# Performance work log

Measured on AMD Instinct MI355X. Metric: run time of the kernel, lower is better.

Reference implementation:

```python
import jax, jax.numpy as jnp
import numpy as np

B, C, H, W = 8, 320, 32, 32
HEADS, DHEAD = 8, 40
CTX_LEN, CTX_DIM = 77, 768
FF_INNER = 4 * C
GROUPS = 32
HW = H * W


def setup_inputs() -> dict:
    key = jax.random.key(0)
    ks = jax.random.split(key, 16)
    def nrm(k, shape, s=0.02):
        return (jax.random.normal(k, shape) * s).astype(jnp.float32)
    z = lambda *s: jnp.zeros(s, jnp.float32)
    o = lambda *s: jnp.ones(s, jnp.float32)
    inp = {}
    inp["x"] = jax.random.normal(ks[0], (B, C, H, W), jnp.float32)
    inp["context"] = jax.random.normal(ks[1], (B, CTX_LEN, CTX_DIM), jnp.float32)
    inp["vis_mask"] = jax.random.uniform(ks[2], (B, HW, HW)) > 0.5
    inp["v2t_mask"] = jax.random.uniform(ks[3], (B, HW, CTX_LEN)) > 0.5
    inp["gn_scale"] = o(C); inp["gn_bias"] = z(C)
    inp["proj_in_w"] = nrm(ks[4], (C, C)); inp["proj_in_b"] = z(C)
    inp["n1_s"] = o(C); inp["n1_b"] = z(C)
    inp["wq1"] = nrm(ks[5], (C, C)); inp["wk1"] = nrm(ks[6], (C, C)); inp["wv1"] = nrm(ks[7], (C, C))
    inp["wo1"] = nrm(ks[8], (C, C)); inp["bo1"] = z(C)
    inp["n2_s"] = o(C); inp["n2_b"] = z(C)
    inp["wq2"] = nrm(ks[9], (C, C)); inp["wk2"] = nrm(ks[10], (CTX_DIM, C)); inp["wv2"] = nrm(ks[11], (CTX_DIM, C))
    inp["wo2"] = nrm(ks[12], (C, C)); inp["bo2"] = z(C)
    inp["n3_s"] = o(C); inp["n3_b"] = z(C)
    inp["ff_w1"] = nrm(ks[13], (C, 2 * FF_INNER)); inp["ff_b1"] = z(2 * FF_INNER)
    inp["ff_w2"] = nrm(ks[14], (FF_INNER, C)); inp["ff_b2"] = z(C)
    inp["proj_out_w"] = nrm(ks[15], (C, C)); inp["proj_out_b"] = z(C)
    return inp


def group_norm(x, scale, bias, eps=1e-6):
    b, c, h, w = x.shape
    xg = x.reshape(b, GROUPS, -1)
    mu = xg.mean(-1, keepdims=True)
    var = xg.var(-1, keepdims=True)
    xn = ((xg - mu) * jax.lax.rsqrt(var + eps)).reshape(b, c, h, w)
    return xn * scale[None, :, None, None] + bias[None, :, None, None]


def layer_norm(x, s, b, eps=1e-5):
    mu = x.mean(-1, keepdims=True)
    var = x.var(-1, keepdims=True)
    return (x - mu) * jax.lax.rsqrt(var + eps) * s + b


def mha(xq, ctx, wq, wk, wv, wo, bo, mask):
    # CrossAttention: manual einsum softmax with boolean mask broadcast over heads
    b, n, _ = xq.shape
    m = ctx.shape[1]
    split = lambda t: t.reshape(b, -1, HEADS, DHEAD).transpose(0, 2, 1, 3)
    q = split(xq @ wq)   # [b,h,n,d]
    k = split(ctx @ wk)  # [b,h,m,d]
    v = split(ctx @ wv)
    sim = jnp.einsum('bhid,bhjd->bhij', q, k) * (DHEAD ** -0.5)
    if mask is not None:
        sim = jnp.where(mask[:, None, :, :], sim, jnp.finfo(sim.dtype).min)
    attn = jax.nn.softmax(sim, axis=-1)
    out = jnp.einsum('bhij,bhjd->bhid', attn, v)
    out = out.transpose(0, 2, 1, 3).reshape(b, n, HEADS * DHEAD)
    return out @ wo + bo


def reference(x, context, vis_mask, v2t_mask, gn_scale, gn_bias, proj_in_w, proj_in_b,
              n1_s, n1_b, wq1, wk1, wv1, wo1, bo1,
              n2_s, n2_b, wq2, wk2, wv2, wo2, bo2,
              n3_s, n3_b, ff_w1, ff_b1, ff_w2, ff_b2,
              proj_out_w, proj_out_b):
    x_in = x
    h = group_norm(x, gn_scale, gn_bias)
    # 1x1 conv proj_in == per-pixel linear; flatten b c h w -> b (hw) c
    h = h.reshape(B, C, HW).transpose(0, 2, 1) @ proj_in_w + proj_in_b
    # masked self-attention (vis mask)
    h = h + mha(layer_norm(h, n1_s, n1_b), layer_norm(h, n1_s, n1_b),
                wq1, wk1, wv1, wo1, bo1, vis_mask)
    # masked cross-attention to text (v2t mask)
    h = h + mha(layer_norm(h, n2_s, n2_b), context,
                wq2, wk2, wv2, wo2, bo2, v2t_mask)
    # GEGLU feedforward (glu=True, mult=4)
    y = layer_norm(h, n3_s, n3_b) @ ff_w1 + ff_b1
    a, g = jnp.split(y, 2, axis=-1)
    h = h + (a * jax.nn.gelu(g, approximate=False)) @ ff_w2 + ff_b2
    # proj_out + residual
    out = (h @ proj_out_w + proj_out_b).transpose(0, 2, 1).reshape(B, C, H, W)
    return out + x_in
```

## Files before the change

### kernel.cpp

```cpp
#include <hip/hip_runtime.h>
#include <hip/hip_bf16.h>
#include <math.h>


#define Bsz   8
#define Cch   320
#define HW    1024
#define NTOK  (Bsz*HW)
#define HEADS 8
#define DHEAD 40
#define CTXL  77
#define CTXD  768
#define FFI   1280
#define MCTX  (Bsz*CTXL)
#define MCTXP 640

typedef unsigned short u16;
typedef unsigned long long u64;
typedef __attribute__((ext_vector_type(8))) u16    u16x8;
typedef __attribute__((ext_vector_type(4))) u16    u16x4;
typedef __attribute__((ext_vector_type(8))) __bf16 bf16x8;
typedef __attribute__((ext_vector_type(4))) float  f32x4;

__device__ inline u16 f2b(float f) {
    unsigned u = __float_as_uint(f);
    return (u16)((u + 0x7FFFu + ((u >> 16) & 1u)) >> 16);
}

__global__ __launch_bounds__(256) void gn_apply(
    const float* __restrict__ x, const float* __restrict__ gnA,
    const float* __restrict__ gnB, u16* __restrict__ out)
{
    __shared__ u16 T[64*72];
    const int tid = threadIdx.x;
    const int c0 = blockIdx.x * 64;
    const int p0 = blockIdx.y * 64;
    const int b  = blockIdx.z;
    for (int e = tid; e < 512; e += 256) {
        int r = e >> 3, ch = e & 7;
        const float* src = x + ((size_t)(b*Cch + c0 + r))*HW + p0 + ch*8;
        float a  = gnA[b*Cch + c0 + r];
        float bb = gnB[b*Cch + c0 + r];
        float4 v0 = *(const float4*)src;
        float4 v1 = *(const float4*)(src + 4);
        u16x8 val;
        val[0] = f2b(v0.x*a + bb); val[1] = f2b(v0.y*a + bb);
        val[2] = f2b(v0.z*a + bb); val[3] = f2b(v0.w*a + bb);
        val[4] = f2b(v1.x*a + bb); val[5] = f2b(v1.y*a + bb);
        val[6] = f2b(v1.z*a + bb); val[7] = f2b(v1.w*a + bb);
        *(u16x8*)&T[r*72 + (ch ^ (r & 7))*8] = val;
    }
    __syncthreads();
    for (int e = tid; e < 4096; e += 256) {
        int p = e >> 6, c = e & 63;
        u16 v = T[c*72 + (((p >> 3) ^ (c & 7))*8) + (p & 7)];
        out[((size_t)(b*HW + p0 + p))*Cch + c0 + c] = v;
    }
}

__global__ __launch_bounds__(256) void layernorm_kernel(
    const float* __restrict__ in, const float* __restrict__ s,
    const float* __restrict__ bgain, u16* __restrict__ out)
{
    int t = blockIdx.x*4 + (threadIdx.x >> 6);
    int lane = threadIdx.x & 63;
    const float* row = in + (size_t)t*Cch;
    float v[5];
    float sum = 0.f, sq = 0.f;
    #pragma unroll
    for (int i = 0; i < 5; ++i) {
        v[i] = row[lane + 64*i];
        sum += v[i]; sq += v[i]*v[i];
    }
    #pragma unroll
    for (int off = 32; off > 0; off >>= 1) {
        sum += __shfl_xor(sum, off);
        sq  += __shfl_xor(sq,  off);
    }
    float mean = sum * (1.f/320.f);
    float var  = sq  * (1.f/320.f) - mean*mean;
    float inv  = rsqrtf(var + 1e-5f);
    u16* orow = out + (size_t)t*Cch;
    #pragma unroll
    for (int i = 0; i < 5; ++i) {
        int c = lane + 64*i;
        orow[c] = f2b((v[i]-mean)*inv*s[c] + bgain[c]);
    }
}

struct WDesc { const float* src; u16* dst; int K; int N; int tiles; float scl; };
struct WPack { WDesc w[12]; };

#define WT_TILES 620
#define CTXBLK   240

__global__ __launch_bounds__(256) void preamble(
    WPack p, const float* __restrict__ ctxsrc, u16* __restrict__ ctxdst,
    const void* __restrict__ vis, const void* __restrict__ v2t,
    u64* __restrict__ bvis, u64* __restrict__ bv2t,
    const float* __restrict__ x, const float* __restrict__ gscale,
    const float* __restrict__ gbias, float* __restrict__ gnA,
    float* __restrict__ gnB)
{
    __shared__ u16 T[64*72];
    int blk = blockIdx.x;
    int tid = threadIdx.x;
    if (blk < WT_TILES) {
        int t = blk;
        #pragma unroll
        for (int i = 0; i < 12; ++i) {
            int nt = p.w[i].tiles;
            if (t < nt) {
                const int K = p.w[i].K, N = p.w[i].N;
                const int ntN = N >> 6;
                const int tk = t / ntN, tn = t - tk*ntN;
                const float scl = p.w[i].scl;
                const float* src = p.w[i].src;
                u16* dst = p.w[i].dst;
                for (int e = tid; e < 512; e += 256) {
                    int r = e >> 3, ch = e & 7;
                    const float* sp = src + (size_t)(tk*64 + r)*N + tn*64 + ch*8;
                    float4 v0 = *(const float4*)sp;
                    float4 v1 = *(const float4*)(sp + 4);
                    u16x8 val;
                    val[0] = f2b(v0.x*scl); val[1] = f2b(v0.y*scl);
                    val[2] = f2b(v0.z*scl); val[3] = f2b(v0.w*scl);
                    val[4] = f2b(v1.x*scl); val[5] = f2b(v1.y*scl);
                    val[6] = f2b(v1.z*scl); val[7] = f2b(v1.w*scl);
                    *(u16x8*)&T[r*72 + (ch ^ (r & 7))*8] = val;
                }
                __syncthreads();
                for (int e = tid; e < 4096; e += 256) {
                    int n = e >> 6, k = e & 63;
                    u16 v = T[k*72 + (((n >> 3) ^ (k & 7))*8) + (n & 7)];
                    dst[(size_t)(tn*64 + n)*K + tk*64 + k] = v;
                }
                return;
            }
            t -= nt;
        }
        return;
    }
    if (blk < WT_TILES + CTXBLK) {
        int idx = (blk - WT_TILES)*2048 + tid*8;
        int r = idx / CTXD;
        u16x8 val = {};
        if (r < MCTX) {
            float4 v0 = *(const float4*)(ctxsrc + idx);
            float4 v1 = *(const float4*)(ctxsrc + idx + 4);
            val[0] = f2b(v0.x); val[1] = f2b(v0.y);
            val[2] = f2b(v0.z); val[3] = f2b(v0.w);
            val[4] = f2b(v1.x); val[5] = f2b(v1.y);
            val[6] = f2b(v1.z); val[7] = f2b(v1.w);
        }
        *(u16x8*)(ctxdst + idx) = val;
        return;
    }
    if (blk >= WT_TILES + CTXBLK + 4096) {
        int gb = blk - (WT_TILES + CTXBLK + 4096);
        int b = gb >> 5, g = gb & 31;
        __shared__ float rs[256], rq[256];
        const float4* xg = (const float4*)(x + ((size_t)b*Cch + g*10)*HW);
        float s = 0.f, q = 0.f;
        #pragma unroll
        for (int i = 0; i < 10; ++i) {
            float4 v = xg[tid + i*256];
            s += v.x + v.y + v.z + v.w;
            q += v.x*v.x + v.y*v.y + v.z*v.z + v.w*v.w;
        }
        rs[tid] = s; rq[tid] = q; __syncthreads();
        for (int off = 128; off > 0; off >>= 1) {
            if (tid < off) { rs[tid] += rs[tid+off]; rq[tid] += rq[tid+off]; }
            __syncthreads();
        }
        if (tid < 10) {
            float mean = rs[0] * (1.f/10240.f);
            float var  = rq[0] * (1.f/10240.f) - mean*mean;
            float inv  = rsqrtf(var + 1e-6f);
            int chn = g*10 + tid;
            float a = inv * gscale[chn];
            gnA[b*Cch + chn] = a;
            gnB[b*Cch + chn] = gbias[chn] - mean*a;
        }
        return;
    }
    __shared__ int any;
    if (tid == 0) any = 0;
    __syncthreads();
    const unsigned char* probe = (const unsigned char*)vis;
    for (int i = tid; i < 4096; i += 256)
        if ((i & 3) && probe[i]) any = 1;
    __syncthreads();
    const int isU8 = any;
    int mb = blk - WT_TILES - CTXBLK;
    const void* mask; u64* bits; int Lkv, nw;
    if (mb < 2048) { mask = vis; bits = bvis; Lkv = HW;   nw = 16; }
    else           { mask = v2t; bits = bv2t; Lkv = CTXL; nw = 2; mb -= 2048; }
    const int wv = tid >> 6, lane = tid & 63;
    const int row = mb*4 + wv;
    const unsigned char* m8  = (const unsigned char*)mask;
    const int*           m32 = (const int*)mask;
    const size_t base = (size_t)row * Lkv;
    for (int w = 0; w < nw; ++w) {
        int j = w*64 + lane;
        bool on = (j < Lkv) && (isU8 ? (m8[base+j] != 0) : (m32[base+j] != 0));
        u64 word = __ballot(on);
        if (lane == 0) bits[(size_t)row*nw + w] = word;
    }
}

__global__ __launch_bounds__(512) void gemm_bf16(
    const u16* __restrict__ A, const u16* __restrict__ Wt,
    const float* __restrict__ bias, const float* __restrict__ res,
    float* __restrict__ out, u16* __restrict__ out_bf, int M, int N, int K)
{
    __shared__ u16 As[2][128*72];
    __shared__ u16 Bs[2][64*72];
    const int tid  = threadIdx.x;
    const int lane = tid & 63;
    const int w    = tid >> 6;
    const int mp   = w >> 1;
    const int np   = w & 1;
    const int m0   = blockIdx.x * 128;
    const int n0   = blockIdx.y * 64;
    const int fr   = lane & 15, fg = lane >> 4;
    const int ar   = tid >> 2, ac = tid & 3;
    const int br   = tid >> 3, bc = tid & 7;

    const u16* pa = A  + (size_t)(m0 + ar)*K + ac*8;
    const u16* pb = Wt + (size_t)(n0 + br)*K + bc*8;
    const int ns = K >> 6;

    *(u16x8*)&As[0][ar*72 + ac*8]      = *(const u16x8*)pa;
    *(u16x8*)&As[0][ar*72 + 32 + ac*8] = *(const u16x8*)(pa + 32);
    *(u16x8*)&Bs[0][br*72 + bc*8]      = *(const u16x8*)pb;
    u16x8 ra0 = {}, ra1 = {}, rb = {};
    if (1 < ns) {
        ra0 = *(const u16x8*)(pa + 64);
        ra1 = *(const u16x8*)(pa + 96);
        rb  = *(const u16x8*)(pb + 64);
    }

    f32x4 acc[2][2] = {};
    for (int s = 0; s < ns; ++s) {
        __syncthreads();
        const int cb = s & 1, nb = cb ^ 1;
        if (s + 1 < ns) {
            *(u16x8*)&As[nb][ar*72 + ac*8]      = ra0;
            *(u16x8*)&As[nb][ar*72 + 32 + ac*8] = ra1;
            *(u16x8*)&Bs[nb][br*72 + bc*8]      = rb;
            if (s + 2 < ns) {
                ra0 = *(const u16x8*)(pa + 64*(s+2));
                ra1 = *(const u16x8*)(pa + 64*(s+2) + 32);
                rb  = *(const u16x8*)(pb + 64*(s+2));
            }
        }
        #pragma unroll
        for (int c = 0; c < 2; ++c) {
            bf16x8 a0 = *(const bf16x8*)&As[cb][(mp*32      + fr)*72 + c*32 + fg*8];
            bf16x8 a1 = *(const bf16x8*)&As[cb][(mp*32 + 16 + fr)*72 + c*32 + fg*8];
            #pragma unroll
            for (int t = 0; t < 2; ++t) {
                bf16x8 b = *(const bf16x8*)&Bs[cb][((np*2+t)*16 + fr)*72 + c*32 + fg*8];
                acc[0][t] = __builtin_amdgcn_mfma_f32_16x16x32_bf16(a0, b, acc[0][t], 0, 0, 0);
                acc[1][t] = __builtin_amdgcn_mfma_f32_16x16x32_bf16(a1, b, acc[1][t], 0, 0, 0);
            }
        }
    }
    #pragma unroll
    for (int at = 0; at < 2; ++at) {
        #pragma unroll
        for (int t = 0; t < 2; ++t) {
            int gn = n0 + (np*2+t)*16 + fr;
            float bv = bias ? bias[gn] : 0.f;
            #pragma unroll
            for (int i = 0; i < 4; ++i) {
                int gm = m0 + mp*32 + at*16 + fg*4 + i;
                float v = acc[at][t][i] + bv;
                if (res) v += res[(size_t)gm*N + gn];
                if (out) out[(size_t)gm*N + gn] = v;
                if (out_bf) out_bf[(size_t)gm*N + gn] = f2b(v);
            }
        }
    }
}

__global__ __launch_bounds__(512) void gemm_qkv_ctx(
    const u16* __restrict__ A, const u16* __restrict__ Wt,
    u16* __restrict__ out_bf, u16* __restrict__ vt_self,
    const u16* __restrict__ ctx, const u16* __restrict__ wk,
    const u16* __restrict__ wv, u16* __restrict__ kout, u16* __restrict__ vout)
{
    __shared__ u16 As[2][128*40];
    __shared__ u16 Bs[2][64*40];
    const int tid  = threadIdx.x;
    const int lane = tid & 63;
    const int w    = tid >> 6;
    const int fr   = lane & 15, fg = lane >> 4;
    const int bi   = blockIdx.x;

    if (bi < 960) {
        const int K  = Cch, N = 960;
        const int m0 = (bi & 63)*128;
        const int n0 = (bi >> 6)*64;
        const int mp = w >> 1, np = w & 1;
        const int ar = tid >> 2, ac = tid & 3;
        const bool hasB = tid < 256;

        const u16* pa = A  + (size_t)(m0 + ar)*K + ac*8;
        const u16* pb = Wt + (size_t)(n0 + ar)*K + ac*8;
        const int nk = K >> 5;

        *(u16x8*)&As[0][ar*40 + ac*8] = *(const u16x8*)pa;
        if (hasB) *(u16x8*)&Bs[0][ar*40 + ac*8] = *(const u16x8*)pb;
        u16x8 xa = *(const u16x8*)(pa + 32);
        u16x8 ya = *(const u16x8*)(pa + 64);
        u16x8 xb = {}, yb = {};
        if (hasB) { xb = *(const u16x8*)(pb + 32); yb = *(const u16x8*)(pb + 64); }

        f32x4 acc[2][2] = {};
        for (int i = 0; i < nk; i += 2) {
            __syncthreads();
            *(u16x8*)&As[1][ar*40 + ac*8] = xa;
            if (hasB) *(u16x8*)&Bs[1][ar*40 + ac*8] = xb;
            if (i + 3 < nk) {
                xa = *(const u16x8*)(pa + 32*(i+3));
                if (hasB) xb = *(const u16x8*)(pb + 32*(i+3));
            }
            {
                bf16x8 a0 = *(const bf16x8*)&As[0][(mp*32      + fr)*40 + fg*8];
                bf16x8 a1 = *(const bf16x8*)&As[0][(mp*32 + 16 + fr)*40 + fg*8];
                #pragma unroll
                for (int t = 0; t < 2; ++t) {
                    bf16x8 b = *(const bf16x8*)&Bs[0][((np*2+t)*16 + fr)*40 + fg*8];
                    acc[0][t] = __builtin_amdgcn_mfma_f32_16x16x32_bf16(a0, b, acc[0][t], 0, 0, 0);
                    acc[1][t] = __builtin_amdgcn_mfma_f32_16x16x32_bf16(a1, b, acc[1][t], 0, 0, 0);
                }
            }
            __syncthreads();
            if (i + 2 < nk) {
                *(u16x8*)&As[0][ar*40 + ac*8] = ya;
                if (hasB) *(u16x8*)&Bs[0][ar*40 + ac*8] = yb;
                if (i + 4 < nk) {
                    ya = *(const u16x8*)(pa + 32*(i+4));
                    if (hasB) yb = *(const u16x8*)(pb + 32*(i+4));
                }
            }
            {
                bf16x8 a0 = *(const bf16x8*)&As[1][(mp*32      + fr)*40 + fg*8];
                bf16x8 a1 = *(const bf16x8*)&As[1][(mp*32 + 16 + fr)*40 + fg*8];
                #pragma unroll
                for (int t = 0; t < 2; ++t) {
                    bf16x8 b = *(const bf16x8*)&Bs[1][((np*2+t)*16 + fr)*40 + fg*8];
                    acc[0][t] = __builtin_amdgcn_mfma_f32_16x16x32_bf16(a0, b, acc[0][t], 0, 0, 0);
                    acc[1][t] = __builtin_amdgcn_mfma_f32_16x16x32_bf16(a1, b, acc[1][t], 0, 0, 0);
                }
            }
        }
        if (n0 < 640) {
            #pragma unroll
            for (int at = 0; at < 2; ++at) {
                #pragma unroll
                for (int t = 0; t < 2; ++t) {
                    int gn = n0 + (np*2+t)*16 + fr;
                    #pragma unroll
                    for (int i = 0; i < 4; ++i) {
                        int gm = m0 + mp*32 + at*16 + fg*4 + i;
                        out_bf[(size_t)gm*N + gn] = f2b(acc[at][t][i]);
                    }
                }
            }
        } else {
            #pragma unroll
            for (int at = 0; at < 2; ++at) {
                #pragma unroll
                for (int t = 0; t < 2; ++t) {
                    int c  = n0 - 640 + (np*2+t)*16 + fr;
                    int gm0 = m0 + mp*32 + at*16 + fg*4;
                    int b  = gm0 >> 10;
                    int p  = gm0 & (HW-1);
                    u16x4 vv;
                    #pragma unroll
                    for (int i = 0; i < 4; ++i) vv[i] = f2b(acc[at][t][i]);
                    *(u16x4*)&vt_self[((size_t)(b*Cch + c))*HW + p] = vv;
                }
            }
        }
        return;
    }

    {
        int cb = bi - 960;
        const int z  = cb / 50; cb -= z*50;
        const int my = cb / 5, nx0 = cb - my*5;
        const int m0 = my*64, n0 = nx0*64;
        const u16* Wt2 = z ? wv : wk;
        u16* outp      = z ? vout : kout;
        const int mg = w >> 1;
        const int np = w & 1;
        const bool isA = tid < 256;
        const int cr = (tid & 255) >> 2, cc = tid & 3;

        const u16* ps = isA ? ctx + (size_t)(m0 + cr)*CTXD + cc*8
                            : Wt2 + (size_t)(n0 + cr)*CTXD + cc*8;
        u16* s0 = isA ? &As[0][cr*40 + cc*8] : &Bs[0][cr*40 + cc*8];
        u16* s1 = isA ? &As[1][cr*40 + cc*8] : &Bs[1][cr*40 + cc*8];
        const int nk = CTXD >> 5;

        *(u16x8*)s0 = *(const u16x8*)ps;
        u16x8 xv = *(const u16x8*)(ps + 32);
        u16x8 yv = *(const u16x8*)(ps + 64);

        f32x4 acc[2] = {};
        for (int i = 0; i < nk; i += 2) {
            __syncthreads();
            *(u16x8*)s1 = xv;
            if (i + 3 < nk) xv = *(const u16x8*)(ps + 32*(i+3));
            {
                bf16x8 a = *(const bf16x8*)&As[0][(mg*16 + fr)*40 + fg*8];
                #pragma unroll
                for (int t = 0; t < 2; ++t) {
                    bf16x8 b = *(const bf16x8*)&Bs[0][((np*2+t)*16 + fr)*40 + fg*8];
                    acc[t] = __builtin_amdgcn_mfma_f32_16x16x32_bf16(a, b, acc[t], 0, 0, 0);
                }
            }
            __syncthreads();
            if (i + 2 < nk) {
                *(u16x8*)s0 = yv;
                if (i + 4 < nk) yv = *(const u16x8*)(ps + 32*(i+4));
            }
            {
                bf16x8 a = *(const bf16x8*)&As[1][(mg*16 + fr)*40 + fg*8];
                #pragma unroll
                for (int t = 0; t < 2; ++t) {
                    bf16x8 b = *(const bf16x8*)&Bs[1][((np*2+t)*16 + fr)*40 + fg*8];
                    acc[t] = __builtin_amdgcn_mfma_f32_16x16x32_bf16(a, b, acc[t], 0, 0, 0);
                }
            }
        }
        #pragma unroll
        for (int t = 0; t < 2; ++t) {
            int gn = n0 + (np*2+t)*16 + fr;
            #pragma unroll
            for (int i = 0; i < 4; ++i) {
                int gm = m0 + mg*16 + fg*4 + i;
                if (gm < MCTX)
                    outp[(size_t)gm*Cch + gn] = f2b(acc[t][i]);
            }
        }
    }
}

__global__ __launch_bounds__(512) void gemm_pout(
    const u16* __restrict__ A, const u16* __restrict__ Wt,
    const float* __restrict__ bias, const float* __restrict__ x,
    float* __restrict__ out, int K)
{
    __shared__ u16 As[2][128*72];
    __shared__ u16 Bs[2][64*72];
    const int tid  = threadIdx.x;
    const int lane = tid & 63;
    const int w    = tid >> 6;
    const int mp   = w >> 1;
    const int np   = w & 1;
    const int m0   = blockIdx.x * 128;
    const int n0   = blockIdx.y * 64;
    const int fr   = lane & 15, fg = lane >> 4;
    const int ar   = tid >> 2, ac = tid & 3;
    const int br   = tid >> 3, bc = tid & 7;

    const u16* pa = A  + (size_t)(m0 + ar)*K + ac*8;
    const u16* pb = Wt + (size_t)(n0 + br)*K + bc*8;
    const int ns = K >> 6;

    *(u16x8*)&As[0][ar*72 + ac*8]      = *(const u16x8*)pa;
    *(u16x8*)&As[0][ar*72 + 32 + ac*8] = *(const u16x8*)(pa + 32);
    *(u16x8*)&Bs[0][br*72 + bc*8]      = *(const u16x8*)pb;
    u16x8 ra0 = {}, ra1 = {}, rb = {};
    if (1 < ns) {
        ra0 = *(const u16x8*)(pa + 64);
        ra1 = *(const u16x8*)(pa + 96);
        rb  = *(const u16x8*)(pb + 64);
    }

    f32x4 acc[2][2] = {};
    for (int s = 0; s < ns; ++s) {
        __syncthreads();
        const int cb = s & 1, nb = cb ^ 1;
        if (s + 1 < ns) {
            *(u16x8*)&As[nb][ar*72 + ac*8]      = ra0;
            *(u16x8*)&As[nb][ar*72 + 32 + ac*8] = ra1;
            *(u16x8*)&Bs[nb][br*72 + bc*8]      = rb;
            if (s + 2 < ns) {
                ra0 = *(const u16x8*)(pa + 64*(s+2));
                ra1 = *(const u16x8*)(pa + 64*(s+2) + 32);
                rb  = *(const u16x8*)(pb + 64*(s+2));
            }
        }
        #pragma unroll
        for (int c = 0; c < 2; ++c) {
            bf16x8 a0 = *(const bf16x8*)&As[cb][(mp*32      + fr)*72 + c*32 + fg*8];
            bf16x8 a1 = *(const bf16x8*)&As[cb][(mp*32 + 16 + fr)*72 + c*32 + fg*8];
            #pragma unroll
            for (int t = 0; t < 2; ++t) {
                bf16x8 b = *(const bf16x8*)&Bs[cb][((np*2+t)*16 + fr)*72 + c*32 + fg*8];
                acc[0][t] = __builtin_amdgcn_mfma_f32_16x16x32_bf16(a0, b, acc[0][t], 0, 0, 0);
                acc[1][t] = __builtin_amdgcn_mfma_f32_16x16x32_bf16(a1, b, acc[1][t], 0, 0, 0);
            }
        }
    }
    #pragma unroll
    for (int at = 0; at < 2; ++at) {
        #pragma unroll
        for (int t = 0; t < 2; ++t) {
            int gn = n0 + (np*2+t)*16 + fr;
            float bv = bias[gn];
            int gm0 = m0 + mp*32 + at*16 + fg*4;
            int b   = gm0 >> 10;
            int pcol= gm0 & (HW-1);
            size_t o = ((size_t)(b*Cch + gn))*HW + pcol;
            f32x4 xv = *(const f32x4*)&x[o];
            f32x4 vv;
            #pragma unroll
            for (int i = 0; i < 4; ++i) vv[i] = acc[at][t][i] + bv + xv[i];
            *(f32x4*)&out[o] = vv;
        }
    }
}

__global__ __launch_bounds__(512) void geglu_bf16(
    const u16* __restrict__ A, const u16* __restrict__ Wt,
    const float* __restrict__ b1, u16* __restrict__ out, int M, int K)
{
    __shared__ u16 As[2][128*40];
    __shared__ u16 Ba[2][64*40];
    __shared__ u16 Bg[2][64*40];
    const int tid  = threadIdx.x;
    const int lane = tid & 63;
    const int w    = tid >> 6;
    const int mp   = w >> 1;
    const int np   = w & 1;
    const int m0   = blockIdx.x * 128;
    const int n0   = blockIdx.y * 64;
    const int fr   = lane & 15, fg = lane >> 4;
    const int ar   = tid >> 2, ac = tid & 3;
    const int nk   = K >> 5;

    const u16* pa = A + (size_t)(m0 + ar)*K + ac*8;
    const int bq = (ar < 64) ? (n0 + ar) : (FFI + n0 + ar - 64);
    const u16* pb = Wt + (size_t)bq*K + ac*8;
    u16* bs0 = (ar < 64) ? &Ba[0][ar*40 + ac*8] : &Bg[0][(ar-64)*40 + ac*8];
    u16* bs1 = (ar < 64) ? &Ba[1][ar*40 + ac*8] : &Bg[1][(ar-64)*40 + ac*8];

    *(u16x8*)&As[0][ar*40 + ac*8] = *(const u16x8*)pa;
    *(u16x8*)bs0 = *(const u16x8*)pb;
    u16x8 xa = *(const u16x8*)(pa + 32);
    u16x8 xb = *(const u16x8*)(pb + 32);
    u16x8 ya = *(const u16x8*)(pa + 64);
    u16x8 yb = *(const u16x8*)(pb + 64);

    f32x4 aca[2][2] = {}, acg[2][2] = {};
    for (int i = 0; i < nk; i += 2) {
        __syncthreads();
        *(u16x8*)&As[1][ar*40 + ac*8] = xa;
        *(u16x8*)bs1 = xb;
        if (i + 3 < nk) {
            xa = *(const u16x8*)(pa + 32*(i+3));
            xb = *(const u16x8*)(pb + 32*(i+3));
        }
        {
            bf16x8 a0 = *(const bf16x8*)&As[0][(mp*32      + fr)*40 + fg*8];
            bf16x8 a1 = *(const bf16x8*)&As[0][(mp*32 + 16 + fr)*40 + fg*8];
            #pragma unroll
            for (int t = 0; t < 2; ++t) {
                bf16x8 ba = *(const bf16x8*)&Ba[0][((np*2+t)*16 + fr)*40 + fg*8];
                bf16x8 bg = *(const bf16x8*)&Bg[0][((np*2+t)*16 + fr)*40 + fg*8];
                aca[0][t] = __builtin_amdgcn_mfma_f32_16x16x32_bf16(a0, ba, aca[0][t], 0, 0, 0);
                aca[1][t] = __builtin_amdgcn_mfma_f32_16x16x32_bf16(a1, ba, aca[1][t], 0, 0, 0);
                acg[0][t] = __builtin_amdgcn_mfma_f32_16x16x32_bf16(a0, bg, acg[0][t], 0, 0, 0);
                acg[1][t] = __builtin_amdgcn_mfma_f32_16x16x32_bf16(a1, bg, acg[1][t], 0, 0, 0);
            }
        }
        __syncthreads();
        if (i + 2 < nk) {
            *(u16x8*)&As[0][ar*40 + ac*8] = ya;
            *(u16x8*)bs0 = yb;
            if (i + 4 < nk) {
                ya = *(const u16x8*)(pa + 32*(i+4));
                yb = *(const u16x8*)(pb + 32*(i+4));
            }
        }
        {
            bf16x8 a0 = *(const bf16x8*)&As[1][(mp*32      + fr)*40 + fg*8];
            bf16x8 a1 = *(const bf16x8*)&As[1][(mp*32 + 16 + fr)*40 + fg*8];
            #pragma unroll
            for (int t = 0; t < 2; ++t) {
                bf16x8 ba = *(const bf16x8*)&Ba[1][((np*2+t)*16 + fr)*40 + fg*8];
                bf16x8 bg = *(const bf16x8*)&Bg[1][((np*2+t)*16 + fr)*40 + fg*8];
                aca[0][t] = __builtin_amdgcn_mfma_f32_16x16x32_bf16(a0, ba, aca[0][t], 0, 0, 0);
                aca[1][t] = __builtin_amdgcn_mfma_f32_16x16x32_bf16(a1, ba, aca[1][t], 0, 0, 0);
                acg[0][t] = __builtin_amdgcn_mfma_f32_16x16x32_bf16(a0, bg, acg[0][t], 0, 0, 0);
                acg[1][t] = __builtin_amdgcn_mfma_f32_16x16x32_bf16(a1, bg, acg[1][t], 0, 0, 0);
            }
        }
    }
    #pragma unroll
    for (int at = 0; at < 2; ++at) {
        #pragma unroll
        for (int t = 0; t < 2; ++t) {
            int gn = n0 + (np*2+t)*16 + fr;
            float ba = b1[gn], bg = b1[FFI + gn];
            #pragma unroll
            for (int i = 0; i < 4; ++i) {
                int gm = m0 + mp*32 + at*16 + fg*4 + i;
                float av = aca[at][t][i] + ba;
                float gv = acg[at][t][i] + bg;
                float gel = 0.5f*gv*(1.f + erff(gv*0.70710678118654752f));
                out[(size_t)gm*FFI + gn] = f2b(av*gel);
            }
        }
    }
}

__global__ __launch_bounds__(512) void flash_mfma(
    const u16* __restrict__ qb, int qstride,
    const u16* __restrict__ kb, int kstride,
    const u16* __restrict__ vt, int vstride,
    const u64* __restrict__ mbits, int nw,
    u16* __restrict__ out,
    int Lkv,
    const u16* __restrict__ tin, u16* __restrict__ tout)
{
    __shared__ u16 QPs[128*72];
    __shared__ u16 Ks[2][64*72];
    __shared__ u16 Vs[2][48*72];

    const int tid  = threadIdx.x;
    const int bi   = blockIdx.x;

    if (bi >= 512) {
        int cb = bi - 512;
        const int c0 = (cb % 5)*64;
        const int t0 = ((cb/5) & 1)*64;
        const int b  = cb/10;
        {
            int r = tid >> 3, ch2 = tid & 7;
            u16x8 val = {};
            if (t0 + r < CTXL)
                val = *(const u16x8*)(tin + ((size_t)(b*CTXL + t0 + r))*Cch + c0 + ch2*8);
            *(u16x8*)&QPs[r*72 + (ch2 ^ (r & 7))*8] = val;
        }
        __syncthreads();
        for (int e = tid; e < 4096; e += 512) {
            int c = e >> 6, t = e & 63;
            u16 v = QPs[t*72 + (((c >> 3) ^ (t & 7))*8) + (c & 7)];
            tout[((size_t)(b*Cch + c0 + c))*128 + t0 + t] = v;
        }
        return;
    }

    const int lane = tid & 63;
    const int w    = tid >> 6;
    const int col  = lane & 15;
    const int quad = lane >> 4;
    const int hb   = (bi & 7)*8 + (bi >> 6);
    const int qt   = (bi >> 3) & 7;
    const int h    = hb & 7;
    const int b    = hb >> 3;
    const int q0   = qt*128;
    const int ch   = tid & 7;
    const int r0   = tid >> 3;

    {
        const u16* qT = qb + ((size_t)(b*HW + q0))*qstride + (size_t)h*DHEAD + ch*8;
        u16x8 v0 = {}, v1 = {};
        if (ch < 5) {
            v0 = *(const u16x8*)(qT + (size_t)r0*qstride);
            v1 = *(const u16x8*)(qT + (size_t)(r0+64)*qstride);
        }
        *(u16x8*)&QPs[r0*72 + ch*8]      = v0;
        *(u16x8*)&QPs[(r0+64)*72 + ch*8] = v1;
    }
    if (tid < 128) {
        int rr  = tid >> 3;
        int row = 40 + (rr & 7);
        int buf = rr >> 3;
        u16x8 v = {};
        if (row == DHEAD) {
            #pragma unroll
            for (int z = 0; z < 8; ++z) v[z] = 0x3F80;
        }
        *(u16x8*)&Vs[buf][row*72 + ch*8] = v;
    }

    const bool kok = ch < 5;
    const u16* kR = kb + (size_t)b*Lkv*kstride + (size_t)h*DHEAD + ch*8
                       + (size_t)r0*kstride;
    const u16* vR = vt + ((size_t)(b*Cch + h*DHEAD))*vstride + ch*8
                       + (size_t)r0*vstride;
    const bool vok = r0 < DHEAD;
    const u64* mrow = mbits + ((size_t)(b*HW + q0 + w*16 + quad*4))*nw;

    u16x8 nk = {}, nv = {};
    if (kok && r0 < Lkv) nk = *(const u16x8*)kR;
    if (vok) nv = *(const u16x8*)vR;

    __syncthreads();
    const bf16x8 qa0 = *(const bf16x8*)&QPs[(w*16 + col)*72 +  0 + quad*8];
    const bf16x8 qa1 = *(const bf16x8*)&QPs[(w*16 + col)*72 + 32 + quad*8];

    f32x4 acc_o[3] = {};

    const int nkt = (Lkv + 63) / 64;
    int cur = 0;
    for (int jt = 0; jt < nkt; ++jt) {
        *(u16x8*)&Ks[cur][r0*72 + ch*8] = nk;
        if (vok) *(u16x8*)&Vs[cur][r0*72 + ch*8] = nv;
        if (jt + 1 < nkt) {
            kR += (size_t)64*kstride;
            vR += 64;
            nk = (u16x8){};
            if (kok && ((jt+1)*64 + r0 < Lkv)) nk = *(const u16x8*)kR;
            if (vok) nv = *(const u16x8*)vR;
        }
        __syncthreads();

        u64 mw[4];
        #pragma unroll
        for (int i = 0; i < 4; ++i) mw[i] = mrow[i*nw + jt];

        f32x4 s[4] = {};
        #pragma unroll
        for (int nt = 0; nt < 4; ++nt) {
            bf16x8 b0 = *(const bf16x8*)&Ks[cur][(nt*16 + col)*72 +  0 + quad*8];
            bf16x8 b1 = *(const bf16x8*)&Ks[cur][(nt*16 + col)*72 + 32 + quad*8];
            s[nt] = __builtin_amdgcn_mfma_f32_16x16x32_bf16(qa0, b0, s[nt], 0, 0, 0);
            s[nt] = __builtin_amdgcn_mfma_f32_16x16x32_bf16(qa1, b1, s[nt], 0, 0, 0);
        }

        #pragma unroll
        for (int i = 0; i < 4; ++i) {
            #pragma unroll
            for (int nt = 0; nt < 4; ++nt) {
                float p = __builtin_amdgcn_exp2f(s[nt][i]);
                unsigned bits = (unsigned)(mw[i] >> (nt*16));
                s[nt][i] = ((bits >> col) & 1u) ? p : 0.f;
            }
        }

        #pragma unroll
        for (int nt = 0; nt < 4; ++nt)
            #pragma unroll
            for (int i = 0; i < 4; ++i)
                QPs[(w*16 + quad*4 + i)*68 + nt*16 + col] =
                    (u16)(__float_as_uint(s[nt][i]) >> 16);

        bf16x8 pa0, pa1;
        __builtin_memcpy(&pa0, &QPs[(w*16 + col)*68 +  0 + quad*8], 16);
        __builtin_memcpy(&pa1, &QPs[(w*16 + col)*68 + 32 + quad*8], 16);
        #pragma unroll
        for (int nt = 0; nt < 3; ++nt) {
            bf16x8 vb0 = *(const bf16x8*)&Vs[cur][(nt*16 + col)*72 +  0 + quad*8];
            bf16x8 vb1 = *(const bf16x8*)&Vs[cur][(nt*16 + col)*72 + 32 + quad*8];
            acc_o[nt] = __builtin_amdgcn_mfma_f32_16x16x32_bf16(pa0, vb0, acc_o[nt], 0, 0, 0);
            acc_o[nt] = __builtin_amdgcn_mfma_f32_16x16x32_bf16(pa1, vb1, acc_o[nt], 0, 0, 0);
        }
        cur ^= 1;
    }

    float inv_l[4];
    #pragma unroll
    for (int i = 0; i < 4; ++i)
        inv_l[i] = 1.f / __shfl(acc_o[2][i], (lane & 48) | 8);

    #pragma unroll
    for (int nt = 0; nt < 3; ++nt) {
        int d = nt*16 + col;
        if (d < DHEAD) {
            #pragma unroll
            for (int i = 0; i < 4; ++i) {
                int q = q0 + w*16 + quad*4 + i;
                out[((size_t)(b*HW + q))*Cch + h*DHEAD + d] = f2b(acc_o[nt][i] * inv_l[i]);
            }
        }
    }
}

extern "C" void kernel_launch(void* const* d_in, const int* in_sizes, int n_in,
                              void* d_out, int out_size, void* d_ws, size_t ws_size,
                              hipStream_t stream)
{
    const float* x        = (const float*)d_in[0];
    const float* context  = (const float*)d_in[1];
    const void*  vis_mask = d_in[2];
    const void*  v2t_mask = d_in[3];
    const float* gn_s     = (const float*)d_in[4];
    const float* gn_b     = (const float*)d_in[5];
    const float* proj_in_w= (const float*)d_in[6];
    const float* proj_in_b= (const float*)d_in[7];
    const float* n1_s     = (const float*)d_in[8];
    const float* n1_b     = (const float*)d_in[9];
    const float* wq1      = (const float*)d_in[10];
    const float* wk1      = (const float*)d_in[11];
    const float* wv1      = (const float*)d_in[12];
    const float* wo1      = (const float*)d_in[13];
    const float* bo1      = (const float*)d_in[14];
    const float* n2_s     = (const float*)d_in[15];
    const float* n2_b     = (const float*)d_in[16];
    const float* wq2      = (const float*)d_in[17];
    const float* wk2      = (const float*)d_in[18];
    const float* wv2      = (const float*)d_in[19];
    const float* wo2      = (const float*)d_in[20];
    const float* bo2      = (const float*)d_in[21];
    const float* n3_s     = (const float*)d_in[22];
    const float* n3_b     = (const float*)d_in[23];
    const float* ff_w1    = (const float*)d_in[24];
    const float* ff_b1    = (const float*)d_in[25];
    const float* ff_w2    = (const float*)d_in[26];
    const float* ff_b2    = (const float*)d_in[27];
    const float* pout_w   = (const float*)d_in[28];
    const float* pout_b   = (const float*)d_in[29];
    float* out = (float*)d_out;

    const size_t TOKC = (size_t)NTOK*Cch;
    float* ws   = (float*)d_ws;
    float* Hb   = ws;
    u16*   QKV  = (u16*)(Hb + TOKC);
    u16*   Vt_g = QKV + 3*TOKC;
    u16*   G_bf = QKV;
    u16*   T0b  = Vt_g + TOKC;
    u16*   T1b  = T0b + TOKC;
    u16*   Hb_bf= T1b + TOKC;
    u16*   Wbf  = Hb_bf + TOKC;
    u64*   mb_vis = (u64*)(Wbf + 2539520);
    u64*   mb_v2t = mb_vis + 131072;
    u16*   ctx_bf = (u16*)(mb_v2t + 16384);
    u16*   Kc_bf  = ctx_bf + MCTXP*CTXD;
    u16*   Vc_bf  = Kc_bf + 640*Cch;
    float* gnA    = (float*)(Vc_bf + 640*Cch);
    float* gnB    = gnA + Bsz*Cch;
    u16*   Vt_x   = (u16*)(gnB + Bsz*Cch);

    u16* w_q1  = Wbf;
    u16* w_k1  = Wbf +  102400;
    u16* w_v1  = Wbf +  204800;
    u16* w_pin = Wbf +  307200;
    u16* w_o1  = Wbf +  409600;
    u16* w_q2  = Wbf +  512000;
    u16* w_o2  = Wbf +  614400;
    u16* w_ff1 = Wbf +  716800;
    u16* w_ff2 = Wbf + 1536000;
    u16* w_po  = Wbf + 1945600;
    u16* w_k2  = Wbf + 2048000;
    u16* w_v2  = Wbf + 2293760;

    const float qscale = 0.15811388300841897f * 1.4426950408889634f;
    WPack pack;
    pack.w[0]  = { wq1,       w_q1,  Cch, Cch, 25,  qscale };
    pack.w[1]  = { wk1,       w_k1,  Cch, Cch, 25,  1.f };
    pack.w[2]  = { wv1,       w_v1,  Cch, Cch, 25,  1.f };
    pack.w[3]  = { proj_in_w, w_pin, Cch, Cch, 25,  1.f };
    pack.w[4]  = { wo1,       w_o1,  Cch, Cch, 25,  1.f };
    pack.w[5]  = { wq2,       w_q2,  Cch, Cch, 25,  qscale };
    pack.w[6]  = { wo2,       w_o2,  Cch, Cch, 25,  1.f };
    pack.w[7]  = { ff_w1,     w_ff1, Cch, 2*FFI, 200, 1.f };
    pack.w[8]  = { ff_w2,     w_ff2, FFI, Cch, 100, 1.f };
    pack.w[9]  = { pout_w,    w_po,  Cch, Cch, 25,  1.f };
    pack.w[10] = { wk2,       w_k2,  CTXD, Cch, 60, 1.f };
    pack.w[11] = { wv2,       w_v2,  CTXD, Cch, 60, 1.f };

    dim3 blk256(256);
    dim3 blk512(512);
    dim3 gTok(NTOK/128, Cch/64);
    dim3 gFF(NTOK/128, FFI/64);
    dim3 gGN(Cch/64, HW/64, Bsz);

    preamble<<<WT_TILES + CTXBLK + 4096 + 256, blk256, 0, stream>>>(
        pack, context, ctx_bf, vis_mask, v2t_mask, mb_vis, mb_v2t,
        x, gn_s, gn_b, gnA, gnB);

    gn_apply<<<gGN, blk256, 0, stream>>>(x, gnA, gnB, T0b);
    gemm_bf16<<<gTok, blk512, 0, stream>>>(T0b, w_pin, proj_in_b, nullptr, Hb, nullptr, NTOK, Cch, Cch);

    layernorm_kernel<<<NTOK/4, blk256, 0, stream>>>(Hb, n1_s, n1_b, T0b);
    gemm_qkv_ctx<<<1060, blk512, 0, stream>>>(T0b, w_q1, QKV, Vt_g,
                                              ctx_bf, w_k2, w_v2, Kc_bf, Vc_bf);
    flash_mfma<<<512 + 80, blk512, 0, stream>>>(QKV, 960, QKV + 320, 960, Vt_g, HW,
                                                mb_vis, 16, T1b, HW, Vc_bf, Vt_x);
    gemm_bf16<<<gTok, blk512, 0, stream>>>(T1b, w_o1, bo1, Hb, Hb, nullptr, NTOK, Cch, Cch);

    layernorm_kernel<<<NTOK/4, blk256, 0, stream>>>(Hb, n2_s, n2_b, T0b);
    gemm_bf16<<<gTok, blk512, 0, stream>>>(T0b, w_q2, nullptr, nullptr, nullptr, QKV, NTOK, Cch, Cch);
    flash_mfma<<<512, blk512, 0, stream>>>(QKV, Cch, Kc_bf, Cch, Vt_x, 128,
                                           mb_v2t, 2, T1b, CTXL, nullptr, nullptr);
    gemm_bf16<<<gTok, blk512, 0, stream>>>(T1b, w_o2, bo2, Hb, Hb, nullptr, NTOK, Cch, Cch);

    layernorm_kernel<<<NTOK/4, blk256, 0, stream>>>(Hb, n3_s, n3_b, T0b);
    geglu_bf16<<<gFF, blk512, 0, stream>>>(T0b, w_ff1, ff_b1, G_bf, NTOK, Cch);
    gemm_bf16<<<gTok, blk512, 0, stream>>>(G_bf, w_ff2, ff_b2, Hb, nullptr, Hb_bf, NTOK, Cch, FFI);

    gemm_pout<<<gTok, blk512, 0, stream>>>(Hb_bf, w_po, pout_b, x, out, Cch);
}
```

Measured before the change: 342.5 us.

## Process two query tiles per block in self-attention flash kernel to reuse K/V

```diff
diff --git a/kernel.cpp b/kernel.cpp
--- a/kernel.cpp
+++ b/kernel.cpp
@@ -622,13 +622,14 @@
     }
 }
 
+template<int NQT>
 __global__ __launch_bounds__(512) void flash_mfma(
     const u16* __restrict__ qb, int qstride,
     const u16* __restrict__ kb, int kstride,
     const u16* __restrict__ vt, int vstride,
     const u64* __restrict__ mbits, int nw,
     u16* __restrict__ out,
-    int Lkv,
+    int Lkv, int natt,
     const u16* __restrict__ tin, u16* __restrict__ tout)
 {
     __shared__ u16 QPs[128*72];
@@ -638,8 +639,8 @@
     const int tid  = threadIdx.x;
     const int bi   = blockIdx.x;
 
-    if (bi >= 512) {
-        int cb = bi - 512;
+    if (bi >= natt) {
+        int cb = bi - natt;
         const int c0 = (cb % 5)*64;
         const int t0 = ((cb/5) & 1)*64;
         const int b  = cb/10;
@@ -663,24 +664,20 @@
     const int w    = tid >> 6;
     const int col  = lane & 15;
     const int quad = lane >> 4;
-    const int hb   = (bi & 7)*8 + (bi >> 6);
-    const int qt   = (bi >> 3) & 7;
-    const int h    = hb & 7;
-    const int b    = hb >> 3;
-    const int q0   = qt*128;
+    int b, h, q0;
+    if (NQT == 2) {
+        b  = bi & 7;
+        h  = bi >> 5;
+        q0 = ((bi >> 3) & 3) * 256;
+    } else {
+        int hb = (bi & 7)*8 + (bi >> 6);
+        h  = hb & 7;
+        b  = hb >> 3;
+        q0 = ((bi >> 3) & 7) * 128;
+    }
     const int ch   = tid & 7;
     const int r0   = tid >> 3;
 
-    {
-        const u16* qT = qb + ((size_t)(b*HW + q0))*qstride + (size_t)h*DHEAD + ch*8;
-        u16x8 v0 = {}, v1 = {};
-        if (ch < 5) {
-            v0 = *(const u16x8*)(qT + (size_t)r0*qstride);
-            v1 = *(const u16x8*)(qT + (size_t)(r0+64)*qstride);
-        }
-        *(u16x8*)&QPs[r0*72 + ch*8]      = v0;
-        *(u16x8*)&QPs[(r0+64)*72 + ch*8] = v1;
-    }
     if (tid < 128) {
         int rr  = tid >> 3;
         int row = 40 + (rr & 7);
@@ -691,6 +688,24 @@
             for (int z = 0; z < 8; ++z) v[z] = 0x3F80;
         }
         *(u16x8*)&Vs[buf][row*72 + ch*8] = v;
+    }
+
+    bf16x8 qa0[NQT], qa1[NQT];
+    #pragma unroll
+    for (int qi = 0; qi < NQT; ++qi) {
+        if (qi) __syncthreads();
+        const u16* qT = qb + ((size_t)(b*HW + q0 + qi*128))*qstride
+                           + (size_t)h*DHEAD + ch*8;
+        u16x8 v0 = {}, v1 = {};
+        if (ch < 5) {
+            v0 = *(const u16x8*)(qT + (size_t)r0*qstride);
+            v1 = *(const u16x8*)(qT + (size_t)(r0+64)*qstride);
+        }
+        *(u16x8*)&QPs[r0*72 + ch*8]      = v0;
+        *(u16x8*)&QPs[(r0+64)*72 + ch*8] = v1;
+        __syncthreads();
+        qa0[qi] = *(const bf16x8*)&QPs[(w*16 + col)*72 +  0 + quad*8];
+        qa1[qi] = *(const bf16x8*)&QPs[(w*16 + col)*72 + 32 + quad*8];
     }
 
     const bool kok = ch < 5;
@@ -705,11 +720,7 @@
     if (kok && r0 < Lkv) nk = *(const u16x8*)kR;
     if (vok) nv = *(const u16x8*)vR;
 
-    __syncthreads();
-    const bf16x8 qa0 = *(const bf16x8*)&QPs[(w*16 + col)*72 +  0 + quad*8];
-    const bf16x8 qa1 = *(const bf16x8*)&QPs[(w*16 + col)*72 + 32 + quad*8];
-
-    f32x4 acc_o[3] = {};
+    f32x4 acc_o[NQT][3] = {};
 
     const int nkt = (Lkv + 63) / 64;
     int cur = 0;
@@ -725,62 +736,72 @@
         }
         __syncthreads();
 
-        u64 mw[4];
-        #pragma unroll
-        for (int i = 0; i < 4; ++i) mw[i] = mrow[i*nw + jt];
-
-        f32x4 s[4] = {};
-        #pragma unroll
-        for (int nt = 0; nt < 4; ++nt) {
-            bf16x8 b0 = *(const bf16x8*)&Ks[cur][(nt*16 + col)*72 +  0 + quad*8];
-            bf16x8 b1 = *(const bf16x8*)&Ks[cur][(nt*16 + col)*72 + 32 + quad*8];
-            s[nt] = __builtin_amdgcn_mfma_f32_16x16x32_bf16(qa0, b0, s[nt], 0, 0, 0);
-            s[nt] = __builtin_amdgcn_mfma_f32_16x16x32_bf16(qa1, b1, s[nt], 0, 0, 0);
-        }
-
-        #pragma unroll
-        for (int i = 0; i < 4; ++i) {
+        u64 mw[NQT][4];
+        #pragma unroll
+        for (int qi = 0; qi < NQT; ++qi)
+            #pragma unroll
+            for (int i = 0; i < 4; ++i)
+                mw[qi][i] = mrow[((size_t)(qi*128 + i))*nw + jt];
+
+        #pragma unroll
+        for (int qi = 0; qi < NQT; ++qi) {
+            f32x4 s[4] = {};
             #pragma unroll
             for (int nt = 0; nt < 4; ++nt) {
-                float p = __builtin_amdgcn_exp2f(s[nt][i]);
-                unsigned bits = (unsigned)(mw[i] >> (nt*16));
-                s[nt][i] = ((bits >> col) & 1u) ? p : 0.f;
-            }
-        }
-
-        #pragma unroll
-        for (int nt = 0; nt < 4; ++nt)
-            #pragma unroll
-            for (int i = 0; i < 4; ++i)
-                QPs[(w*16 + quad*4 + i)*68 + nt*16 + col] =
-                    (u16)(__float_as_uint(s[nt][i]) >> 16);
-
-        bf16x8 pa0, pa1;
-        __builtin_memcpy(&pa0, &QPs[(w*16 + col)*68 +  0 + quad*8], 16);
-        __builtin_memcpy(&pa1, &QPs[(w*16 + col)*68 + 32 + quad*8], 16);
+                bf16x8 b0 = *(const bf16x8*)&Ks[cur][(nt*16 + col)*72 +  0 + quad*8];
+                bf16x8 b1 = *(const bf16x8*)&Ks[cur][(nt*16 + col)*72 + 32 + quad*8];
+                s[nt] = __builtin_amdgcn_mfma_f32_16x16x32_bf16(qa0[qi], b0, s[nt], 0, 0, 0);
+                s[nt] = __builtin_amdgcn_mfma_f32_16x16x32_bf16(qa1[qi], b1, s[nt], 0, 0, 0);
+            }
+
+            #pragma unroll
+            for (int i = 0; i < 4; ++i) {
+                #pragma unroll
+                for (int nt = 0; nt < 4; ++nt) {
+                    float p = __builtin_amdgcn_exp2f(s[nt][i]);
+                    unsigned bits = (unsigned)(mw[qi][i] >> (nt*16));
+                    s[nt][i] = ((bits >> col) & 1u) ? p : 0.f;
+                }
+            }
+
+            #pragma unroll
+            for (int nt = 0; nt < 4; ++nt)
+                #pragma unroll
+                for (int i = 0; i < 4; ++i)
+                    QPs[(w*16 + quad*4 + i)*68 + nt*16 + col] =
+                        (u16)(__float_as_uint(s[nt][i]) >> 16);
+
+            bf16x8 pa0, pa1;
+            __builtin_memcpy(&pa0, &QPs[(w*16 + col)*68 +  0 + quad*8], 16);
+            __builtin_memcpy(&pa1, &QPs[(w*16 + col)*68 + 32 + quad*8], 16);
+            #pragma unroll
+            for (int nt = 0; nt < 3; ++nt) {
+                bf16x8 vb0 = *(const bf16x8*)&Vs[cur][(nt*16 + col)*72 +  0 + quad*8];
+                bf16x8 vb1 = *(const bf16x8*)&Vs[cur][(nt*16 + col)*72 + 32 + quad*8];
+                acc_o[qi][nt] = __builtin_amdgcn_mfma_f32_16x16x32_bf16(pa0, vb0, acc_o[qi][nt], 0, 0, 0);
+                acc_o[qi][nt] = __builtin_amdgcn_mfma_f32_16x16x32_bf16(pa1, vb1, acc_o[qi][nt], 0, 0, 0);
+            }
+        }
+        cur ^= 1;
+    }
+
+    #pragma unroll
+    for (int qi = 0; qi < NQT; ++qi) {
+        float inv_l[4];
+        #pragma unroll
+        for (int i = 0; i < 4; ++i)
+            inv_l[i] = 1.f / __shfl(acc_o[qi][2][i], (lane & 48) | 8);
+
         #pragma unroll
         for (int nt = 0; nt < 3; ++nt) {
-            bf16x8 vb0 = *(const bf16x8*)&Vs[cur][(nt*16 + col)*72 +  0 + quad*8];
-            bf16x8 vb1 = *(const bf16x8*)&Vs[cur][(nt*16 + col)*72 + 32 + quad*8];
-            acc_o[nt] = __builtin_amdgcn_mfma_f32_16x16x32_bf16(pa0, vb0, acc_o[nt], 0, 0, 0);
-            acc_o[nt] = __builtin_amdgcn_mfma_f32_16x16x32_bf16(pa1, vb1, acc_o[nt], 0, 0, 0);
-        }
-        cur ^= 1;
-    }
-
-    float inv_l[4];
-    #pragma unroll
-    for (int i = 0; i < 4; ++i)
-        inv_l[i] = 1.f / __shfl(acc_o[2][i], (lane & 48) | 8);
-
-    #pragma unroll
-    for (int nt = 0; nt < 3; ++nt) {
-        int d = nt*16 + col;
-        if (d < DHEAD) {
-            #pragma unroll
-            for (int i = 0; i < 4; ++i) {
-                int q = q0 + w*16 + quad*4 + i;
-                out[((size_t)(b*HW + q))*Cch + h*DHEAD + d] = f2b(acc_o[nt][i] * inv_l[i]);
+            int d = nt*16 + col;
+            if (d < DHEAD) {
+                #pragma unroll
+                for (int i = 0; i < 4; ++i) {
+                    int q = q0 + qi*128 + w*16 + quad*4 + i;
+                    out[((size_t)(b*HW + q))*Cch + h*DHEAD + d] =
+                        f2b(acc_o[qi][nt][i] * inv_l[i]);
+                }
             }
         }
     }
@@ -885,14 +906,14 @@
     layernorm_kernel<<<NTOK/4, blk256, 0, stream>>>(Hb, n1_s, n1_b, T0b);
     gemm_qkv_ctx<<<1060, blk512, 0, stream>>>(T0b, w_q1, QKV, Vt_g,
                                               ctx_bf, w_k2, w_v2, Kc_bf, Vc_bf);
-    flash_mfma<<<512 + 80, blk512, 0, stream>>>(QKV, 960, QKV + 320, 960, Vt_g, HW,
-                                                mb_vis, 16, T1b, HW, Vc_bf, Vt_x);
+    flash_mfma<2><<<256 + 80, blk512, 0, stream>>>(QKV, 960, QKV + 320, 960, Vt_g, HW,
+                                                   mb_vis, 16, T1b, HW, 256, Vc_bf, Vt_x);
     gemm_bf16<<<gTok, blk512, 0, stream>>>(T1b, w_o1, bo1, Hb, Hb, nullptr, NTOK, Cch, Cch);
 
     layernorm_kernel<<<NTOK/4, blk256, 0, stream>>>(Hb, n2_s, n2_b, T0b);
     gemm_bf16<<<gTok, blk512, 0, stream>>>(T0b, w_q2, nullptr, nullptr, nullptr, QKV, NTOK, Cch, Cch);
-    flash_mfma<<<512, blk512, 0, stream>>>(QKV, Cch, Kc_bf, Cch, Vt_x, 128,
-                                           mb_v2t, 2, T1b, CTXL, nullptr, nullptr);
+    flash_mfma<1><<<512, blk512, 0, stream>>>(QKV, Cch, Kc_bf, Cch, Vt_x, 128,
+                                              mb_v2t, 2, T1b, CTXL, 512, nullptr, nullptr);
     gemm_bf16<<<gTok, blk512, 0, stream>>>(T1b, w_o2, bo2, Hb, Hb, nullptr, NTOK, Cch, Cch);
 
     layernorm_kernel<<<NTOK/4, blk256, 0, stream>>>(Hb, n3_s, n3_b, T0b);
```

Result: no change. 345.7 us (+0.9%).
